# Performance work log

Measured on AMD Instinct MI355X. Metric: run time of the kernel, lower is better.

## Reference

```python
import jax, jax.numpy as jnp
import numpy as np

# static config (matches init_kwargs)
P = 16          # proj_patch_dim (window size)
F = 128         # fmap_dim
NH = F // P     # windows per side = 8
N = P * P       # tokens per window = 256
H = 8           # attn_heads
A = 32          # attn_dim (head dim)
C = 32          # leff_filters_out (channels)
INNER = 128     # leff_filters
B = 8           # batch
EPS = 1e-5

# relative-position index (static)
_c = np.stack(np.meshgrid(np.arange(P), np.arange(P), indexing='ij'))  # [2,P,P]
_f = _c.reshape(2, -1)                                                  # [2,N]
_r = _f[:, :, None] - _f[:, None, :]                                    # [2,N,N]
_rpi = (_r[0] + P - 1) * (2 * P - 1) + (_r[1] + P - 1)                  # [N,N]
RPI = jnp.asarray(_rpi.reshape(-1))

# shifted-window attention mask (static)
_sm = np.zeros((F, F), np.float32)
_cnt = 0
_slices = (slice(0, -P), slice(-P, -P // 2), slice(-P // 2, None))
for _hs in _slices:
    for _ws in _slices:
        _sm[_hs, _ws] = _cnt
        _cnt += 1
_smw = _sm.reshape(NH, P, NH, P).transpose(0, 2, 1, 3).reshape(NH * NH, N)
_am = _smw[:, None, :] - _smw[:, :, None]
_am = np.where(_am != 0, np.float32(-100.0), np.float32(0.0))
SHIFT_MASK = jnp.asarray(_am.reshape(1, NH * NH, 1, N, N))


def _ln(x, g, b):
    m = jnp.mean(x, axis=-1, keepdims=True)
    v = jnp.var(x, axis=-1, keepdims=True)
    return (x - m) / jnp.sqrt(v + EPS) * g + b


def setup_inputs() -> dict:
    key = jax.random.key(0)
    ks = jax.random.split(key, 16)
    s = 0.02
    return {
        'x': jax.random.normal(ks[0], (B, F * F, C), jnp.float32),
        'norm1_g': jnp.ones((C,), jnp.float32),
        'norm1_b': jnp.zeros((C,), jnp.float32),
        'mod_w': jax.random.normal(ks[1], (N, C), jnp.float32) * s,
        'qkv_w': jax.random.normal(ks[2], (C, 3 * H * A), jnp.float32) * s,
        'qkv_b': jnp.zeros((3 * H * A,), jnp.float32),
        'rpbt': jax.random.normal(ks[3], ((2 * P - 1) ** 2, H), jnp.float32) * s,
        'rev_w': jax.random.normal(ks[4], (H * A, C), jnp.float32) * s,
        'rev_b': jnp.zeros((C,), jnp.float32),
        'norm2_g': jnp.ones((C,), jnp.float32),
        'norm2_b': jnp.zeros((C,), jnp.float32),
        'lp1_w': jax.random.normal(ks[5], (C, INNER), jnp.float32) * s,
        'lp1_b': jnp.zeros((INNER,), jnp.float32),
        'conv_w': jax.random.normal(ks[6], (3, 3, INNER, INNER), jnp.float32) * s,  # HWIO
        'conv_b': jnp.zeros((INNER,), jnp.float32),
        'lp2_w': jax.random.normal(ks[7], (INNER, C), jnp.float32) * s,
        'lp2_b': jnp.zeros((C,), jnp.float32),
    }


def reference(x, norm1_g, norm1_b, mod_w, qkv_w, qkv_b, rpbt, rev_w, rev_b,
              norm2_g, norm2_b, lp1_w, lp1_b, conv_w, conv_b, lp2_w, lp2_b):
    shortcut = x
    h = _ln(x, norm1_g, norm1_b)
    h = h.reshape(B, F, F, C)
    h = jnp.roll(h, (-P // 2, -P // 2), axis=(1, 2))          # cyclic shift
    # window partition: [B*NH*NH, N, C]
    h = h.reshape(B, NH, P, NH, P, C).transpose(0, 1, 3, 2, 4, 5).reshape(B * NH * NH, N, C)
    h = h + mod_w                                              # learned modulator
    qkv = h @ qkv_w + qkv_b                                    # [W, N, 3*H*A]
    qkv = qkv.reshape(-1, N, 3, H, A).transpose(2, 0, 3, 1, 4) # [3, W, H, N, A]
    q = qkv[0] * (A ** -0.5)
    k = qkv[1]
    v = qkv[2]
    attn = jnp.einsum('whna,whma->whnm', q, k)                 # [W, H, N, N]
    rpb = rpbt[RPI].reshape(N, N, H).transpose(2, 0, 1)        # [H, N, N]
    attn = attn + rpb[None]
    attn = attn.reshape(B, NH * NH, H, N, N) + SHIFT_MASK
    attn = attn.reshape(-1, H, N, N)
    attn = jax.nn.softmax(attn, axis=-1)
    o = jnp.einsum('whnm,whma->whna', attn, v)                 # [W, H, N, A]
    o = o.transpose(0, 2, 1, 3).reshape(-1, N, H * A)
    o = o @ rev_w + rev_b                                      # [W, N, C]
    # window reverse + reverse cyclic shift
    o = o.reshape(B, NH, NH, P, P, C).transpose(0, 1, 3, 2, 4, 5).reshape(B, F, F, C)
    o = jnp.roll(o, (P // 2, P // 2), axis=(1, 2)).reshape(B, F * F, C)
    x_res = shortcut + o
    # LeFF
    y = _ln(x_res, norm2_g, norm2_b)
    y = jax.nn.gelu(y @ lp1_w + lp1_b, approximate=False)
    y = y.reshape(B, F, F, INNER)
    y = jax.lax.conv_general_dilated(y, conv_w, (1, 1), 'SAME',
                                     dimension_numbers=('NHWC', 'HWIO', 'NHWC')) + conv_b
    y = jax.nn.gelu(y, approximate=False)
    y = y.reshape(B, F * F, INNER)
    y = jax.nn.gelu(y @ lp2_w + lp2_b, approximate=False)
    return y + x_res
```

## Files before the change

kernel.cpp:

```cpp
#include <hip/hip_runtime.h>
#include <math.h>

#define Fdim 128
#define Pw   16
#define Hh   8
#define Cc   32
#define Bb   8

typedef short  short8  __attribute__((ext_vector_type(8)));
typedef float  floatx4 __attribute__((ext_vector_type(4)));

#define QSCL   0.2550348637f
#define MASKC2 (-144.26950408889634f)

__device__ __forceinline__ float gelu_f(float x){
    return 0.5f * x * (1.0f + erff(x * 0.70710678118654752f));
}
__device__ __forceinline__ unsigned pk2(float a, float b){
    unsigned ua = __builtin_bit_cast(unsigned, a) + 0x8000u;
    unsigned ub = __builtin_bit_cast(unsigned, b) + 0x8000u;
    return __builtin_amdgcn_perm(ub, ua, 0x07060302);
}
__device__ __forceinline__ unsigned pk2t(float a, float b){
    return __builtin_amdgcn_perm(__builtin_bit_cast(unsigned, b),
                                 __builtin_bit_cast(unsigned, a), 0x07060302);
}
__device__ __forceinline__ short bf16s(float a){
    return (short)((__builtin_bit_cast(unsigned, a) + 0x8000u) >> 16);
}
__device__ __forceinline__ float hi2f(unsigned d){ return __builtin_bit_cast(float, d & 0xffff0000u); }
__device__ __forceinline__ float lo2f(unsigned d){ return __builtin_bit_cast(float, d << 16); }

__global__ __launch_bounds__(256) void prep_kernel(
    const float* __restrict__ qkv_w, const float* __restrict__ rev_w,
    const float* __restrict__ rpbt,  const float* __restrict__ lp1_w,
    const float* __restrict__ conv_w, const float* __restrict__ lp2_w,
    short* __restrict__ qkv_wT, short* __restrict__ rev_wT, unsigned* __restrict__ rplb,
    short* __restrict__ lp1_wT, short* __restrict__ conv_wT, short* __restrict__ lp2_wT)
{
    int i = blockIdx.x * 256 + threadIdx.x;
    if (i < 24576){
        int col = i >> 5, c = i & 31;
        qkv_wT[i] = bf16s(qkv_w[c*768 + col]);
    } else if (i < 32768){
        int j = i - 24576;
        int h = j >> 10, r = j & 1023;
        int c = r >> 5, a = r & 31;
        rev_wT[j] = bf16s(rev_w[(h*32 + a)*32 + c]);
    } else if (i < 40464){
        int j = i - 32768;
        int h = j / 962, d = j % 962;
        int g0 = (d < 481) ? (2*d) : (2*(d-481) + 1);
        float f0 = (g0     < 961) ? rpbt[g0*8 + h]*1.4426950408889634f : 0.f;
        float f1 = (g0 + 1 < 961) ? rpbt[(g0+1)*8 + h]*1.4426950408889634f : 0.f;
        rplb[j] = pk2(f0, f1);
    } else if (i < 44560){
        int j = i - 40464;
        int f = j >> 5, c = j & 31;
        lp1_wT[j] = bf16s(lp1_w[c*128 + f]);
    } else if (i < 192016){
        int j = i - 44560;
        int ci_in = j & 7;
        int co    = (j >> 3) & 127;
        int chk   = (j >> 10) & 3;
        int s     = j >> 12;
        int tap = s % 9, kc = s / 9;
        conv_wT[j] = bf16s(conv_w[(tap*128 + kc*32 + chk*8 + ci_in)*128 + co]);
    } else if (i < 196112){
        int j = i - 192016;
        int oc = j >> 7, co = j & 127;
        lp2_wT[j] = bf16s(lp2_w[co*32 + oc]);
    }
}

__global__
__attribute__((amdgpu_flat_work_group_size(512,512), amdgpu_waves_per_eu(4,4)))
void attn_kernel(
    const float* __restrict__ x,   const float* __restrict__ n1g,
    const float* __restrict__ n1b, const float* __restrict__ mod_w,
    const float* __restrict__ qkv_b, const float* __restrict__ rev_b,
    const short* __restrict__ qkv_wT, const short* __restrict__ rev_wT,
    const unsigned* __restrict__ rplb,
    float* __restrict__ x_res)
{
    __shared__ __align__(16) short hmodS[4*256*8];
    __shared__ __align__(16) short Kbuf[256*40];
    __shared__ __align__(16) short Qbuf[256*40];
    __shared__ __align__(16) short VTb[32*264];
    __shared__ __align__(16) unsigned rplbS[962];
    __shared__ unsigned regnp[64];

    const int w  = blockIdx.x;
    const int b  = w >> 6;
    const int wi = w & 63;
    const int wh = wi >> 3, ww = wi & 7;
    const int tid  = threadIdx.x;
    const int wv   = tid >> 6;
    const int ln   = tid & 63;
    const int quad = ln >> 4;
    const int l15  = ln & 15;
    const bool masked = (wh == 7) || (ww == 7);

    if (tid < 256){
        const int n  = tid;
        const int rn = n >> 4, cn = n & 15;
        const int gh = (wh*Pw + rn + 8) & 127;
        const int gw = (ww*Pw + cn + 8) & 127;
        const float* xr = x + (((size_t)b << 14) + (gh << 7) + gw) * Cc;
        float v[Cc];
        const float4* x4 = reinterpret_cast<const float4*>(xr);
        float4* v4 = reinterpret_cast<float4*>(v);
        #pragma unroll
        for (int i = 0; i < Cc/4; i++) v4[i] = x4[i];
        float mean = 0.f;
        #pragma unroll
        for (int c = 0; c < Cc; c++) mean += v[c];
        mean *= (1.0f/Cc);
        float var = 0.f;
        #pragma unroll
        for (int c = 0; c < Cc; c++){ float d = v[c] - mean; var = fmaf(d, d, var); }
        var *= (1.0f/Cc);
        const float rinv = rsqrtf(var + 1e-5f);
        #pragma unroll
        for (int c = 0; c < Cc; c++)
            v[c] = (v[c] - mean)*rinv*n1g[c] + n1b[c] + mod_w[n*Cc + c];
        #pragma unroll
        for (int i = 0; i < 4; i++){
            uint4 dw;
            dw.x = pk2(v[8*i+0], v[8*i+1]);
            dw.y = pk2(v[8*i+2], v[8*i+3]);
            dw.z = pk2(v[8*i+4], v[8*i+5]);
            dw.w = pk2(v[8*i+6], v[8*i+7]);
            *(uint4*)(&hmodS[i*2048 + n*8]) = dw;
        }
    }
    if (tid < 64){
        int rm  = tid >> 2;
        int shm = wh*Pw + rm;
        int hreg = (shm < 112) ? 0 : ((shm < 120) ? 1 : 2);
        unsigned dw = 0;
        #pragma unroll
        for (int i = 0; i < 4; i++){
            int cm  = (tid & 3)*4 + i;
            int swm = ww*Pw + cm;
            int wreg = (swm < 112) ? 0 : ((swm < 120) ? 1 : 2);
            dw |= (unsigned)(hreg*3 + wreg) << (8*i);
        }
        regnp[tid] = dw;
    }
    __syncthreads();

    unsigned regq[2] = {0,0};
    if (masked){
        #pragma unroll
        for (int nt = 0; nt < 2; nt++){
            int q = wv*32 + nt*16 + l15;
            regq[nt] = (regnp[q >> 2] >> ((q & 3)*8)) & 255u;
        }
    }

    floatx4 RV[2][2];
    #pragma unroll
    for (int cm = 0; cm < 2; cm++)
        #pragma unroll
        for (int nt = 0; nt < 2; nt++)
            RV[cm][nt] = (floatx4){0.f,0.f,0.f,0.f};

    const int s0lane = 12 + l15 - 4*quad;
    const floatx4 zz = (floatx4){0.f,0.f,0.f,0.f};
    const short8 ONEv = {0x3F80,0x3F80,0x3F80,0x3F80,0x3F80,0x3F80,0x3F80,0x3F80};

    for (int h = 0; h < Hh; h++){
        __syncthreads();

        #pragma unroll
        for (int k2 = 0; k2 < 2; k2++){
            int i = k2*512 + tid;
            if (i < 962) rplbS[i] = rplb[h*962 + i];
        }

        short8 HF[2];
        #pragma unroll
        for (int ii = 0; ii < 2; ii++)
            HF[ii] = *(const short8*)(&hmodS[quad*2048 + (wv*32 + ii*16 + l15)*8]);
        short8 WQ[2], WK[2], WVb[2];
        float4 bq[2], bk[2]; float bv[2];
        #pragma unroll
        for (int mt = 0; mt < 2; mt++){
            WQ[mt]  = *(const short8*)(qkv_wT + (      h*32 + mt*16 + l15)*32 + quad*8);
            WK[mt]  = *(const short8*)(qkv_wT + (256 + h*32 + mt*16 + l15)*32 + quad*8);
            WVb[mt] = *(const short8*)(qkv_wT + (512 + h*32 + mt*16 + l15)*32 + quad*8);
            bq[mt]  = *(const float4*)(qkv_b +       h*32 + mt*16 + quad*4);
            bk[mt]  = *(const float4*)(qkv_b + 256 + h*32 + mt*16 + quad*4);
            bv[mt]  = qkv_b[512 + h*32 + mt*16 + l15];
        }
        #pragma unroll
        for (int ii = 0; ii < 2; ii++){
            const int tok = wv*32 + ii*16;
            #pragma unroll
            for (int mt = 0; mt < 2; mt++){
                floatx4 qf = __builtin_amdgcn_mfma_f32_16x16x32_bf16(WQ[mt], HF[ii], zz, 0,0,0);
                floatx4 kf = __builtin_amdgcn_mfma_f32_16x16x32_bf16(WK[mt], HF[ii], zz, 0,0,0);
                floatx4 vf = __builtin_amdgcn_mfma_f32_16x16x32_bf16(HF[ii], WVb[mt], zz, 0,0,0);
                uint2 qv;
                qv.x = pk2((qf[0]+bq[mt].x)*QSCL, (qf[1]+bq[mt].y)*QSCL);
                qv.y = pk2((qf[2]+bq[mt].z)*QSCL, (qf[3]+bq[mt].w)*QSCL);
                *(uint2*)(&Qbuf[(tok + l15)*40 + mt*16 + quad*4]) = qv;
                uint2 kv;
                kv.x = pk2(kf[0]+bk[mt].x, kf[1]+bk[mt].y);
                kv.y = pk2(kf[2]+bk[mt].z, kf[3]+bk[mt].w);
                *(uint2*)(&Kbuf[(tok + l15)*40 + mt*16 + quad*4]) = kv;
                uint2 vv;
                vv.x = pk2(vf[0]+bv[mt], vf[1]+bv[mt]);
                vv.y = pk2(vf[2]+bv[mt], vf[3]+bv[mt]);
                *(uint2*)(&VTb[(mt*16 + l15)*264 + tok + quad*4]) = vv;
            }
        }
        __syncthreads();

        short8 QB[2];
        #pragma unroll
        for (int nt = 0; nt < 2; nt++)
            QB[nt] = *(const short8*)(&Qbuf[(wv*32 + nt*16 + l15)*40 + quad*8]);

        floatx4 OT[2][2];
        #pragma unroll
        for (int am = 0; am < 2; am++)
            #pragma unroll
            for (int nt = 0; nt < 2; nt++)
                OT[am][nt] = (floatx4){0.f,0.f,0.f,0.f};
        floatx4 RS[2] = {zz, zz};

        for (int ch = 0; ch < 8; ch++){
            short8 KA[2];
            KA[0] = *(const short8*)(&Kbuf[(ch*32 +      l15)*40 + quad*8]);
            KA[1] = *(const short8*)(&Kbuf[(ch*32 + 16 + l15)*40 + quad*8]);

            unsigned pd0[3], pd1[3];
            int base = wv*2 - ch*2;
            #pragma unroll
            for (int j = 0; j < 3; j++){
                int dt  = base + j - 1;
                int g0  = (dt + 15)*31 + s0lane;
                int dwi = (g0 & 1) ? (481 + (g0 >> 1)) : (g0 >> 1);
                pd0[j] = rplbS[dwi];
                pd1[j] = rplbS[dwi + 1];
            }
            unsigned rk[2] = {0,0};
            if (masked){
                rk[0] = regnp[ch*8 +     quad];
                rk[1] = regnp[ch*8 + 4 + quad];
            }

            #pragma unroll
            for (int sub = 0; sub < 2; sub++){
                #pragma unroll
                for (int nt = 0; nt < 2; nt++){
                    int j = nt - sub + 1;
                    floatx4 ci;
                    ci[0] = hi2f(pd1[j]); ci[1] = lo2f(pd1[j]);
                    ci[2] = hi2f(pd0[j]); ci[3] = lo2f(pd0[j]);
                    if (masked){
                        ci[0] += (((rk[sub]      ) & 255u) == regq[nt]) ? 0.f : MASKC2;
                        ci[1] += (((rk[sub] >>  8) & 255u) == regq[nt]) ? 0.f : MASKC2;
                        ci[2] += (((rk[sub] >> 16) & 255u) == regq[nt]) ? 0.f : MASKC2;
                        ci[3] += (((rk[sub] >> 24) & 255u) == regq[nt]) ? 0.f : MASKC2;
                    }
                    floatx4 S = __builtin_amdgcn_mfma_f32_16x16x32_bf16(KA[sub], QB[nt], ci, 0,0,0);
                    float p0 = __builtin_amdgcn_exp2f(S[0]);
                    float p1 = __builtin_amdgcn_exp2f(S[1]);
                    float p2 = __builtin_amdgcn_exp2f(S[2]);
                    float p3 = __builtin_amdgcn_exp2f(S[3]);
                    uint2 pv; pv.x = pk2t(p0, p1); pv.y = pk2t(p2, p3);
                    *(uint2*)(&Qbuf[(wv*32 + nt*16 + l15)*40 + sub*16 + quad*4]) = pv;
                }
            }

            short8 VA0 = *(const short8*)(&VTb[(     l15)*264 + ch*32 + quad*8]);
            short8 VA1 = *(const short8*)(&VTb[(16 + l15)*264 + ch*32 + quad*8]);
            #pragma unroll
            for (int nt = 0; nt < 2; nt++){
                short8 PB = *(const short8*)(&Qbuf[(wv*32 + nt*16 + l15)*40 + quad*8]);
                OT[0][nt] = __builtin_amdgcn_mfma_f32_16x16x32_bf16(VA0, PB, OT[0][nt], 0,0,0);
                OT[1][nt] = __builtin_amdgcn_mfma_f32_16x16x32_bf16(VA1, PB, OT[1][nt], 0,0,0);
                RS[nt]    = __builtin_amdgcn_mfma_f32_16x16x32_bf16(ONEv, PB, RS[nt], 0,0,0);
            }
        }

        float inv[2];
        inv[0] = 1.0f / RS[0][0];
        inv[1] = 1.0f / RS[1][0];
        #pragma unroll
        for (int am = 0; am < 2; am++)
            #pragma unroll
            for (int nt = 0; nt < 2; nt++){
                floatx4 o = OT[am][nt];
                float iv = inv[nt];
                uint2 ov;
                ov.x = pk2(o[0]*iv, o[1]*iv);
                ov.y = pk2(o[2]*iv, o[3]*iv);
                *(uint2*)(&Qbuf[(wv*32 + nt*16 + l15)*40 + am*16 + quad*4]) = ov;
            }

        short8 RA0 = *(const short8*)(rev_wT + h*1024 + (     l15)*32 + quad*8);
        short8 RA1 = *(const short8*)(rev_wT + h*1024 + (16 + l15)*32 + quad*8);
        #pragma unroll
        for (int nt = 0; nt < 2; nt++){
            short8 OB = *(const short8*)(&Qbuf[(wv*32 + nt*16 + l15)*40 + quad*8]);
            RV[0][nt] = __builtin_amdgcn_mfma_f32_16x16x32_bf16(RA0, OB, RV[0][nt], 0,0,0);
            RV[1][nt] = __builtin_amdgcn_mfma_f32_16x16x32_bf16(RA1, OB, RV[1][nt], 0,0,0);
        }
    }

    #pragma unroll
    for (int cm = 0; cm < 2; cm++){
        float4 rb = *(const float4*)(rev_b + cm*16 + quad*4);
        #pragma unroll
        for (int nt = 0; nt < 2; nt++){
            int gh = (wh*Pw + wv*2 + nt + 8) & 127;
            int gw = (ww*Pw + l15 + 8) & 127;
            size_t gaddr = (((size_t)b << 14) + (gh << 7) + gw)*Cc + cm*16 + quad*4;
            float4 xv = *(const float4*)(x + gaddr);
            floatx4 o = RV[cm][nt];
            float4 ov;
            ov.x = xv.x + rb.x + o[0];
            ov.y = xv.y + rb.y + o[1];
            ov.z = xv.z + rb.z + o[2];
            ov.w = xv.w + rb.w + o[3];
            *(float4*)(x_res + gaddr) = ov;
        }
    }
}

__global__
__attribute__((amdgpu_flat_work_group_size(512,512), amdgpu_waves_per_eu(4,4)))
void leff_kernel(
    const float* __restrict__ x_res, const float* __restrict__ n2g,
    const float* __restrict__ n2b,  const float* __restrict__ lp1_b,
    const float* __restrict__ conv_b, const float* __restrict__ lp2_b,
    const short* __restrict__ lp1_wT, const short* __restrict__ conv_wT,
    const short* __restrict__ lp2_wT, float* __restrict__ out)
{
    __shared__ __align__(16) char lds[70144];
    short* xa   = (short*)lds;
    short* y1c  = (short*)(lds + 26880);
    short* wbuf = (short*)(lds + 53760);
    short* y2   = (short*)lds;

    const int blk = blockIdx.x;
    const int b   = blk >> 6;
    const int ty  = (blk >> 3) & 7, tx = blk & 7;
    const int tid  = threadIdx.x;
    const int wv   = tid >> 6;
    const int ln   = tid & 63;
    const int quad = ln >> 4;
    const int l15  = ln & 15;
    const floatx4 zz = (floatx4){0.f,0.f,0.f,0.f};

    if (tid < 336){
        int hp = tid;
        int hy = hp / 18, hx = hp - hy*18;
        int gy = ty*16 + hy - 1, gx = tx*16 + hx - 1;
        bool ok = (hp < 324) && ((unsigned)gy < 128u) && ((unsigned)gx < 128u);
        if (ok){
            const float* xr = x_res + (((size_t)b << 14) + (gy << 7) + gx)*Cc;
            float v[Cc];
            const float4* x4 = reinterpret_cast<const float4*>(xr);
            float4* v4 = reinterpret_cast<float4*>(v);
            #pragma unroll
            for (int i = 0; i < Cc/4; i++) v4[i] = x4[i];
            float mean = 0.f;
            #pragma unroll
            for (int c = 0; c < Cc; c++) mean += v[c];
            mean *= (1.0f/Cc);
            float var = 0.f;
            #pragma unroll
            for (int c = 0; c < Cc; c++){ float d = v[c] - mean; var = fmaf(d, d, var); }
            var *= (1.0f/Cc);
            const float rinv = rsqrtf(var + 1e-5f);
            #pragma unroll
            for (int i = 0; i < 4; i++){
                float w0 = (v[8*i+0]-mean)*rinv*n2g[8*i+0] + n2b[8*i+0];
                float w1 = (v[8*i+1]-mean)*rinv*n2g[8*i+1] + n2b[8*i+1];
                float w2 = (v[8*i+2]-mean)*rinv*n2g[8*i+2] + n2b[8*i+2];
                float w3 = (v[8*i+3]-mean)*rinv*n2g[8*i+3] + n2b[8*i+3];
                float w4 = (v[8*i+4]-mean)*rinv*n2g[8*i+4] + n2b[8*i+4];
                float w5 = (v[8*i+5]-mean)*rinv*n2g[8*i+5] + n2b[8*i+5];
                float w6 = (v[8*i+6]-mean)*rinv*n2g[8*i+6] + n2b[8*i+6];
                float w7 = (v[8*i+7]-mean)*rinv*n2g[8*i+7] + n2b[8*i+7];
                uint4 dw;
                dw.x = pk2(w0,w1); dw.y = pk2(w2,w3);
                dw.z = pk2(w4,w5); dw.w = pk2(w6,w7);
                *(uint4*)(xa + hp*40 + i*8) = dw;
            }
        } else {
            uint4 z = {0,0,0,0};
            #pragma unroll
            for (int i = 0; i < 4; i++) *(uint4*)(xa + hp*40 + i*8) = z;
        }
    }

    ((uint4*)wbuf)[tid] = ((const uint4*)conv_wT)[tid];

    floatx4 acc[2][8];
    #pragma unroll
    for (int j = 0; j < 2; j++)
        #pragma unroll
        for (int m = 0; m < 8; m++) acc[j][m] = zz;

    for (int idx = 0; idx < 36; idx++){
        const int kc  = idx / 9;
        const int tap = idx - kc*9;

        if (tap == 0){
            __syncthreads();
            short8 A1[2]; float4 b1[2];
            #pragma unroll
            for (int mt = 0; mt < 2; mt++){
                A1[mt] = *(const short8*)(lp1_wT + (kc*32 + mt*16 + l15)*32 + quad*8);
                b1[mt] = *(const float4*)(lp1_b + kc*32 + mt*16 + quad*4);
            }
            #pragma unroll
            for (int ii = 0; ii < 3; ii++){
                int nt = wv + 8*ii;
                if (nt < 21){
                    int px = nt*16 + l15;
                    int hy = px / 18, hx = px - hy*18;
                    int gy = ty*16 + hy - 1, gx = tx*16 + hx - 1;
                    bool oob = (px >= 324) || ((unsigned)gy > 127u) || ((unsigned)gx > 127u);
                    short8 Bx = *(const short8*)(xa + px*40 + quad*8);
                    #pragma unroll
                    for (int mt = 0; mt < 2; mt++){
                        floatx4 c = __builtin_amdgcn_mfma_f32_16x16x32_bf16(A1[mt], Bx, zz, 0,0,0);
                        float v0 = oob ? 0.f : gelu_f(c[0] + b1[mt].x);
                        float v1 = oob ? 0.f : gelu_f(c[1] + b1[mt].y);
                        float v2 = oob ? 0.f : gelu_f(c[2] + b1[mt].z);
                        float v3 = oob ? 0.f : gelu_f(c[3] + b1[mt].w);
                        uint2 pv; pv.x = pk2(v0, v1); pv.y = pk2(v2, v3);
                        *(uint2*)(y1c + px*40 + mt*16 + quad*4) = pv;
                    }
                }
            }
        }

        uint4 pf;
        if (idx < 35) pf = ((const uint4*)conv_wT)[(idx + 1)*512 + tid];

        __syncthreads();

        const short* wb = wbuf + (idx & 1)*4096;
        const int ky = tap / 3, kx = tap - ky*3;

        short8 Bf[2];
        #pragma unroll
        for (int j = 0; j < 2; j++){
            int oy = wv*2 + j;
            int hp = (oy + ky)*18 + kx + l15;
            Bf[j] = *(const short8*)(y1c + hp*40 + quad*8);
        }
        #pragma unroll
        for (int m = 0; m < 8; m++){
            short8 Aw = *(const short8*)(wb + quad*1024 + (m*16 + l15)*8);
            acc[0][m] = __builtin_amdgcn_mfma_f32_16x16x32_bf16(Aw, Bf[0], acc[0][m], 0,0,0);
            acc[1][m] = __builtin_amdgcn_mfma_f32_16x16x32_bf16(Aw, Bf[1], acc[1][m], 0,0,0);
        }

        if (idx < 35)
            ((uint4*)(wbuf + ((idx + 1) & 1)*4096))[tid] = pf;
    }

    __syncthreads();

    #pragma unroll
    for (int j = 0; j < 2; j++){
        int px = (wv*2 + j)*16 + l15;
        #pragma unroll
        for (int m = 0; m < 8; m++){
            float4 cb = *(const float4*)(conv_b + m*16 + quad*4);
            floatx4 a = acc[j][m];
            float v0 = gelu_f(a[0] + cb.x);
            float v1 = gelu_f(a[1] + cb.y);
            float v2 = gelu_f(a[2] + cb.z);
            float v3 = gelu_f(a[3] + cb.w);
            uint2 pv; pv.x = pk2(v0, v1); pv.y = pk2(v2, v3);
            *(uint2*)(y2 + px*136 + m*16 + quad*4) = pv;
        }
    }
    __syncthreads();

    short8 A2[2][4]; float4 lb[2];
    #pragma unroll
    for (int mt = 0; mt < 2; mt++){
        #pragma unroll
        for (int k = 0; k < 4; k++)
            A2[mt][k] = *(const short8*)(lp2_wT + (mt*16 + l15)*128 + k*32 + quad*8);
        lb[mt] = *(const float4*)(lp2_b + mt*16 + quad*4);
    }
    #pragma unroll
    for (int j = 0; j < 2; j++){
        int oy = wv*2 + j;
        floatx4 c2[2] = {zz, zz};
        #pragma unroll
        for (int k = 0; k < 4; k++){
            short8 Bf = *(const short8*)(y2 + (oy*16 + l15)*136 + k*32 + quad*8);
            c2[0] = __builtin_amdgcn_mfma_f32_16x16x32_bf16(A2[0][k], Bf, c2[0], 0,0,0);
            c2[1] = __builtin_amdgcn_mfma_f32_16x16x32_bf16(A2[1][k], Bf, c2[1], 0,0,0);
        }
        int gy = ty*16 + oy, gx = tx*16 + l15;
        size_t base = (((size_t)b << 14) + (gy << 7) + gx)*Cc;
        #pragma unroll
        for (int mt = 0; mt < 2; mt++){
            size_t ad = base + mt*16 + quad*4;
            float4 xr = *(const float4*)(x_res + ad);
            float4 ov;
            ov.x = gelu_f(c2[mt][0] + lb[mt].x) + xr.x;
            ov.y = gelu_f(c2[mt][1] + lb[mt].y) + xr.y;
            ov.z = gelu_f(c2[mt][2] + lb[mt].z) + xr.z;
            ov.w = gelu_f(c2[mt][3] + lb[mt].w) + xr.w;
            *(float4*)(out + ad) = ov;
        }
    }
}

extern "C" void kernel_launch(void* const* d_in, const int* in_sizes, int n_in,
                              void* d_out, int out_size, void* d_ws, size_t ws_size,
                              hipStream_t stream)
{
    (void)in_sizes; (void)n_in; (void)out_size; (void)ws_size;
    const float* x      = (const float*)d_in[0];
    const float* n1g    = (const float*)d_in[1];
    const float* n1b    = (const float*)d_in[2];
    const float* mod_w  = (const float*)d_in[3];
    const float* qkv_w  = (const float*)d_in[4];
    const float* qkv_b  = (const float*)d_in[5];
    const float* rpbt   = (const float*)d_in[6];
    const float* rev_w  = (const float*)d_in[7];
    const float* rev_b  = (const float*)d_in[8];
    const float* n2g    = (const float*)d_in[9];
    const float* n2b    = (const float*)d_in[10];
    const float* lp1_w  = (const float*)d_in[11];
    const float* lp1_b  = (const float*)d_in[12];
    const float* conv_w = (const float*)d_in[13];
    const float* conv_b = (const float*)d_in[14];
    const float* lp2_w  = (const float*)d_in[15];
    const float* lp2_b  = (const float*)d_in[16];
    float* out = (float*)d_out;

    char* wsb = (char*)d_ws;
    float*    x_res  = (float*)wsb;
    short*    qkv_wT = (short*)(wsb + 16777216);
    short*    rev_wT = (short*)(wsb + 16826368);
    unsigned* rplbT  = (unsigned*)(wsb + 16842752);
    short*    lp1_wT = (short*)(wsb + 16873536);
    short*    conv_wT= (short*)(wsb + 16881728);
    short*    lp2_wT = (short*)(wsb + 17176640);

    prep_kernel<<<767, 256, 0, stream>>>(qkv_w, rev_w, rpbt, lp1_w, conv_w, lp2_w,
                                         qkv_wT, rev_wT, rplbT, lp1_wT, conv_wT, lp2_wT);
    attn_kernel<<<512, 512, 0, stream>>>(x, n1g, n1b, mod_w, qkv_b, rev_b,
                                         qkv_wT, rev_wT, rplbT, x_res);
    leff_kernel<<<512, 512, 0, stream>>>(x_res, n2g, n2b, lp1_b, conv_b, lp2_b,
                                         lp1_wT, conv_wT, lp2_wT, out);
}
```

Measured before the change: 245.4 us.

## Fold V projection into output projection per head to drop rev matmul

```diff
diff --git a/kernel.cpp b/kernel.cpp
--- a/kernel.cpp
+++ b/kernel.cpp
@@ -35,8 +35,10 @@
     const float* __restrict__ qkv_w, const float* __restrict__ rev_w,
     const float* __restrict__ rpbt,  const float* __restrict__ lp1_w,
     const float* __restrict__ conv_w, const float* __restrict__ lp2_w,
+    const float* __restrict__ qkv_b, const float* __restrict__ rev_b,
     short* __restrict__ qkv_wT, short* __restrict__ rev_wT, unsigned* __restrict__ rplb,
-    short* __restrict__ lp1_wT, short* __restrict__ conv_wT, short* __restrict__ lp2_wT)
+    short* __restrict__ lp1_wT, short* __restrict__ conv_wT, short* __restrict__ lp2_wT,
+    short* __restrict__ wvr, float* __restrict__ rbtot)
 {
     int i = blockIdx.x * 256 + threadIdx.x;
     if (i < 24576){
@@ -70,6 +72,19 @@
         int j = i - 192016;
         int oc = j >> 7, co = j & 127;
         lp2_wT[j] = bf16s(lp2_w[co*32 + oc]);
+    } else if (i < 204304){
+        int j  = i - 196112;
+        int h  = j >> 10, aa = (j >> 5) & 31, c = j & 31;
+        float s = 0.f;
+        for (int a = 0; a < 32; a++)
+            s += qkv_w[c*768 + 512 + h*32 + a] * rev_w[(h*32 + a)*32 + aa];
+        wvr[j] = bf16s(s);
+    } else if (i < 204336){
+        int aa = i - 204304;
+        float s = rev_b[aa];
+        for (int m = 0; m < 256; m++)
+            s += qkv_b[512 + m] * rev_w[m*32 + aa];
+        rbtot[aa] = s;
     }
 }
 
@@ -78,8 +93,8 @@
 void attn_kernel(
     const float* __restrict__ x,   const float* __restrict__ n1g,
     const float* __restrict__ n1b, const float* __restrict__ mod_w,
-    const float* __restrict__ qkv_b, const float* __restrict__ rev_b,
-    const short* __restrict__ qkv_wT, const short* __restrict__ rev_wT,
+    const float* __restrict__ qkv_b, const float* __restrict__ rbtot,
+    const short* __restrict__ qkv_wT, const short* __restrict__ wvr,
     const unsigned* __restrict__ rplb,
     float* __restrict__ x_res)
 {
@@ -184,15 +199,14 @@
         for (int ii = 0; ii < 2; ii++)
             HF[ii] = *(const short8*)(&hmodS[quad*2048 + (wv*32 + ii*16 + l15)*8]);
         short8 WQ[2], WK[2], WVb[2];
-        float4 bq[2], bk[2]; float bv[2];
+        float4 bq[2], bk[2];
         #pragma unroll
         for (int mt = 0; mt < 2; mt++){
             WQ[mt]  = *(const short8*)(qkv_wT + (      h*32 + mt*16 + l15)*32 + quad*8);
             WK[mt]  = *(const short8*)(qkv_wT + (256 + h*32 + mt*16 + l15)*32 + quad*8);
-            WVb[mt] = *(const short8*)(qkv_wT + (512 + h*32 + mt*16 + l15)*32 + quad*8);
+            WVb[mt] = *(const short8*)(wvr    + (      h*32 + mt*16 + l15)*32 + quad*8);
             bq[mt]  = *(const float4*)(qkv_b +       h*32 + mt*16 + quad*4);
             bk[mt]  = *(const float4*)(qkv_b + 256 + h*32 + mt*16 + quad*4);
-            bv[mt]  = qkv_b[512 + h*32 + mt*16 + l15];
         }
         #pragma unroll
         for (int ii = 0; ii < 2; ii++){
@@ -211,8 +225,8 @@
                 kv.y = pk2(kf[2]+bk[mt].z, kf[3]+bk[mt].w);
                 *(uint2*)(&Kbuf[(tok + l15)*40 + mt*16 + quad*4]) = kv;
                 uint2 vv;
-                vv.x = pk2(vf[0]+bv[mt], vf[1]+bv[mt]);
-                vv.y = pk2(vf[2]+bv[mt], vf[3]+bv[mt]);
+                vv.x = pk2(vf[0], vf[1]);
+                vv.y = pk2(vf[2], vf[3]);
                 *(uint2*)(&VTb[(mt*16 + l15)*264 + tok + quad*4]) = vv;
             }
         }
@@ -296,25 +310,16 @@
             for (int nt = 0; nt < 2; nt++){
                 floatx4 o = OT[am][nt];
                 float iv = inv[nt];
-                uint2 ov;
-                ov.x = pk2(o[0]*iv, o[1]*iv);
-                ov.y = pk2(o[2]*iv, o[3]*iv);
-                *(uint2*)(&Qbuf[(wv*32 + nt*16 + l15)*40 + am*16 + quad*4]) = ov;
-            }
-
-        short8 RA0 = *(const short8*)(rev_wT + h*1024 + (     l15)*32 + quad*8);
-        short8 RA1 = *(const short8*)(rev_wT + h*1024 + (16 + l15)*32 + quad*8);
-        #pragma unroll
-        for (int nt = 0; nt < 2; nt++){
-            short8 OB = *(const short8*)(&Qbuf[(wv*32 + nt*16 + l15)*40 + quad*8]);
-            RV[0][nt] = __builtin_amdgcn_mfma_f32_16x16x32_bf16(RA0, OB, RV[0][nt], 0,0,0);
-            RV[1][nt] = __builtin_amdgcn_mfma_f32_16x16x32_bf16(RA1, OB, RV[1][nt], 0,0,0);
-        }
+                RV[am][nt][0] = fmaf(o[0], iv, RV[am][nt][0]);
+                RV[am][nt][1] = fmaf(o[1], iv, RV[am][nt][1]);
+                RV[am][nt][2] = fmaf(o[2], iv, RV[am][nt][2]);
+                RV[am][nt][3] = fmaf(o[3], iv, RV[am][nt][3]);
+            }
     }
 
     #pragma unroll
     for (int cm = 0; cm < 2; cm++){
-        float4 rb = *(const float4*)(rev_b + cm*16 + quad*4);
+        float4 rb = *(const float4*)(rbtot + cm*16 + quad*4);
         #pragma unroll
         for (int nt = 0; nt < 2; nt++){
             int gh = (wh*Pw + wv*2 + nt + 8) & 127;
@@ -554,11 +559,15 @@
     short*    lp1_wT = (short*)(wsb + 16873536);
     short*    conv_wT= (short*)(wsb + 16881728);
     short*    lp2_wT = (short*)(wsb + 17176640);
-
-    prep_kernel<<<767, 256, 0, stream>>>(qkv_w, rev_w, rpbt, lp1_w, conv_w, lp2_w,
-                                         qkv_wT, rev_wT, rplbT, lp1_wT, conv_wT, lp2_wT);
-    attn_kernel<<<512, 512, 0, stream>>>(x, n1g, n1b, mod_w, qkv_b, rev_b,
-                                         qkv_wT, rev_wT, rplbT, x_res);
+    short*    wvrT   = (short*)(wsb + 17184832);
+    float*    rbtot  = (float*)(wsb + 17201216);
+
+    prep_kernel<<<799, 256, 0, stream>>>(qkv_w, rev_w, rpbt, lp1_w, conv_w, lp2_w,
+                                         qkv_b, rev_b,
+                                         qkv_wT, rev_wT, rplbT, lp1_wT, conv_wT, lp2_wT,
+                                         wvrT, rbtot);
+    attn_kernel<<<512, 512, 0, stream>>>(x, n1g, n1b, mod_w, qkv_b, rbtot,
+                                         qkv_wT, wvrT, rplbT, x_res);
     leff_kernel<<<512, 512, 0, stream>>>(x_res, n2g, n2b, lp1_b, conv_b, lp2_b,
                                          lp1_wT, conv_wT, lp2_wT, out);
 }
```

Measured after the change: 250.7 us. 2.2% more time.
